# Performance work log

Measured on AMD Instinct MI355X. Metric: run time of the kernel, lower is better.

Reference implementation:

```python
import jax, jax.numpy as jnp
import numpy as np


def rotate_half(x):
    d = x.shape[-1] // 2
    return jnp.concatenate([-x[..., d:], x[..., :d]], axis=-1)


def setup_inputs() -> dict:
    key = jax.random.key(0)
    ks = jax.random.split(key, 8)
    B, T, C, H = 2, 2048, 2048, 16
    hd = C // H
    x = jax.random.normal(ks[0], (B, T, C), dtype=jnp.float32)
    # realistic RoPE tables
    inv_freq = 1.0 / (10000.0 ** (jnp.arange(0, hd, 2, dtype=jnp.float32) / hd))
    t = jnp.arange(T, dtype=jnp.float32)
    freqs = jnp.einsum('t,f->tf', t, inv_freq)
    emb = jnp.concatenate([freqs, freqs], axis=-1)  # [T, hd]
    cos = jnp.cos(emb)
    sin = jnp.sin(emb)
    mask = jnp.tril(jnp.ones((T, T), dtype=bool))[None, None]  # causal [1,1,T,T]
    s = C ** -0.5
    Wq = jax.random.normal(ks[1], (C, C), dtype=jnp.float32) * s
    Wk = jax.random.normal(ks[2], (C, C), dtype=jnp.float32) * s
    Wv = jax.random.normal(ks[3], (C, C), dtype=jnp.float32) * s
    Wo = jax.random.normal(ks[4], (C, C), dtype=jnp.float32) * s
    return {"x": x, "cos": cos, "sin": sin, "mask": mask,
            "Wq": Wq, "Wk": Wk, "Wv": Wv, "Wo": Wo}


def reference(x, cos, sin, mask, Wq, Wk, Wv, Wo):
    B, T, C = x.shape
    H = 16
    hd = C // H
    scale = hd ** -0.5
    # projections: torch Linear stores W as [out,in], y = x @ W^T
    def proj(W):
        return jnp.einsum('btc,dc->btd', x, W).reshape(B, T, H, hd).transpose(0, 2, 1, 3)
    q, k, v = proj(Wq), proj(Wk), proj(Wv)  # [B,H,T,hd]
    c = cos[None, None]  # [1,1,T,hd]
    s = sin[None, None]
    q = q * c + rotate_half(q) * s
    k = k * c + rotate_half(k) * s
    attn = jnp.einsum('bhqd,bhkd->bhqk', q, k) * scale
    attn = jnp.where(mask, attn, -jnp.inf)
    attn = jax.nn.softmax(attn, axis=-1)
    out = jnp.einsum('bhqk,bhkd->bhqd', attn, v)
    out = out.transpose(0, 2, 1, 3).reshape(B, T, C)
    return jnp.einsum('btc,dc->btd', out, Wo)
```

## Files before the change

kernel.cpp:

```cpp
#include <hip/hip_runtime.h>
#include <cstdint>

typedef __bf16 bf16_t;
typedef __bf16 bf16x8 __attribute__((ext_vector_type(8)));
typedef __bf16 bf16x4 __attribute__((ext_vector_type(4)));
typedef float  f32x4  __attribute__((ext_vector_type(4)));

#define BB 2
#define TT 2048
#define CC 2048
#define HH 16
#define HD 128

static __device__ __forceinline__ void async_copy16(const void* gp, void* lp) {
  __builtin_amdgcn_global_load_lds(
      (const __attribute__((address_space(1))) void*)(uintptr_t)gp,
      (__attribute__((address_space(3))) void*)(uint32_t)(uintptr_t)lp,
      16, 0, 0);
}

__global__ __launch_bounds__(256)
void cast_all(const float* __restrict__ x, const float* __restrict__ wq,
              const float* __restrict__ wk, const float* __restrict__ wv,
              const float* __restrict__ wo, bf16_t* __restrict__ xb,
              bf16_t* __restrict__ wq_b) {
  const int NX4 = (BB * TT * CC) / 4;
  const int NW4 = (CC * CC) / 4;
  int i = blockIdx.x * 256 + threadIdx.x;
  const float* s;
  bf16_t* d;
  int off;
  if (i < NX4) {
    s = x; d = xb; off = i;
  } else {
    int j = i - NX4;
    int w = j >> 20;
    off = j & (NW4 - 1);
    s = (w == 0) ? wq : (w == 1) ? wk : (w == 2) ? wv : wo;
    d = wq_b + (size_t)w * (CC * CC);
  }
  float4 v = ((const float4*)s)[off];
  bf16x4 o;
  o[0] = (bf16_t)v.x; o[1] = (bf16_t)v.y; o[2] = (bf16_t)v.z; o[3] = (bf16_t)v.w;
  ((bf16x4*)d)[off] = o;
}

template <int MODE>
__global__ __launch_bounds__(256)
void gemm_bt(const bf16_t* __restrict__ A, const bf16_t* __restrict__ Bw,
             void* __restrict__ C0, void* __restrict__ C1, void* __restrict__ C2,
             int Kdim, int Ndim) {
  __shared__ __align__(16) char smem[128 * 136 * 2];
  bf16_t* As = (bf16_t*)smem;
  bf16_t* Bs = (bf16_t*)(smem + 16384);
  const int tid  = threadIdx.x;
  const int wave = tid >> 6, lane = tid & 63;
  const int quad = lane >> 4, l16 = lane & 15;
  const int m0 = blockIdx.y * 128, n0 = blockIdx.x * 128;
  const int wm = (wave >> 1) * 64, wn = (wave & 1) * 64;

  f32x4 acc[4][4] = {};

  const int srow = lane >> 3;
  const int scol = (((lane & 7) ^ srow) & 7) * 8;
  const int swz  = (l16 & 7) * 8;

  for (int k0 = 0; k0 < Kdim; k0 += 64) {
#pragma unroll
    for (int i = 0; i < 4; ++i) {
      int chunk = wave * 4 + i;
      int row = chunk * 8 + srow;
      async_copy16(A + (size_t)(m0 + row) * Kdim + k0 + scol, As + chunk * 512);
    }
#pragma unroll
    for (int i = 0; i < 4; ++i) {
      int chunk = wave * 4 + i;
      int row = chunk * 8 + srow;
      async_copy16(Bw + (size_t)(n0 + row) * Kdim + k0 + scol, Bs + chunk * 512);
    }
    __syncthreads();
#pragma unroll
    for (int kk = 0; kk < 64; kk += 32) {
      const int koff = (kk + quad * 8) ^ swz;
      bf16x8 af[4], bfr[4];
#pragma unroll
      for (int i = 0; i < 4; ++i)
        af[i] = *(const bf16x8*)&As[(wm + i * 16 + l16) * 64 + koff];
#pragma unroll
      for (int j = 0; j < 4; ++j)
        bfr[j] = *(const bf16x8*)&Bs[(wn + j * 16 + l16) * 64 + koff];
#pragma unroll
      for (int i = 0; i < 4; ++i)
#pragma unroll
        for (int j = 0; j < 4; ++j)
          acc[i][j] = __builtin_amdgcn_mfma_f32_16x16x32_bf16(af[i], bfr[j], acc[i][j], 0, 0, 0);
    }
    __syncthreads();
  }

  if (MODE == 0) {
#pragma unroll
    for (int i = 0; i < 4; ++i)
#pragma unroll
      for (int j = 0; j < 4; ++j) {
        int gcol = n0 + wn + j * 16 + l16;
#pragma unroll
        for (int r = 0; r < 4; ++r) {
          int grow = m0 + wm + i * 16 + quad * 4 + r;
          ((float*)C0)[(size_t)grow * Ndim + gcol] = acc[i][j][r];
        }
      }
  } else {
    const int h = (n0 & (CC - 1)) >> 7;
    bf16_t* Ct = (bf16_t*)smem;
    __syncthreads();
#pragma unroll
    for (int i = 0; i < 4; ++i)
#pragma unroll
      for (int j = 0; j < 4; ++j) {
        int c = wn + j * 16 + l16;
#pragma unroll
        for (int r = 0; r < 4; ++r)
          Ct[(wm + i * 16 + quad * 4 + r) * 136 + c] = (bf16_t)acc[i][j][r];
      }
    __syncthreads();
    const unsigned short* Cu = (const unsigned short*)Ct;
    int col = tid >> 1;
    int rh  = (tid & 1) * 64;
    int grow0 = m0 + rh;
    int b = grow0 >> 11, t0 = grow0 & (TT - 1);
    unsigned int pk[32];
#pragma unroll
    for (int s = 0; s < 32; ++s) {
      unsigned int lo = Cu[(rh + 2 * s) * 136 + col];
      unsigned int hi = Cu[(rh + 2 * s + 1) * 136 + col];
      pk[s] = lo | (hi << 16);
    }
    bf16_t* dstp = (bf16_t*)C2 + ((size_t)(b * HH + h) * HD + col) * TT + t0;
#pragma unroll
    for (int u = 0; u < 8; ++u) {
      uint4 w; w.x = pk[4*u]; w.y = pk[4*u+1]; w.z = pk[4*u+2]; w.w = pk[4*u+3];
      *(uint4*)(dstp + 8 * u) = w;
    }
  }
}

__global__ __launch_bounds__(512, 2)
void gemm_qkv256(const bf16_t* __restrict__ A, const bf16_t* __restrict__ Bw,
                 bf16_t* __restrict__ Qo, bf16_t* __restrict__ Ko,
                 const float* __restrict__ cosT, const float* __restrict__ sinT,
                 int Kdim) {
  extern __shared__ __align__(16) char smem[];
  bf16_t* lds = (bf16_t*)smem;
  const int tid  = threadIdx.x;
  const int wave = tid >> 6, lane = tid & 63;
  const int quad = lane >> 4, l16 = lane & 15;
  const int wm = wave >> 2, wn = wave & 3;
  const int n0 = blockIdx.x * 256, m0 = blockIdx.y * 256;

  const int srow = lane >> 3;
  const int scol = ((lane & 7) ^ srow) * 8;
  const int swz  = (l16 & 7) * 8;
  const int nK = Kdim >> 6;

  const bf16_t* Ag = A  + (size_t)(m0 + wave * 32 + srow) * Kdim + scol;
  const bf16_t* Bg = Bw + (size_t)(n0 + wave * 32 + srow) * Kdim + scol;
  const int ldsChunk = wave * 4 * 512;

#define STAGE_A(kt, buf)                                                      \
  {                                                                           \
    bf16_t* dstA = lds + (buf) * 32768 + ldsChunk;                            \
    const bf16_t* srcA = Ag + (kt) * 64;                                      \
    _Pragma("unroll")                                                         \
    for (int ci = 0; ci < 4; ++ci)                                            \
      async_copy16(srcA + (size_t)(ci * 8) * Kdim, dstA + ci * 512);          \
  }
#define STAGE_B(kt, buf)                                                      \
  {                                                                           \
    bf16_t* dstB = lds + (buf) * 32768 + 16384 + ldsChunk;                    \
    const bf16_t* srcB = Bg + (kt) * 64;                                      \
    _Pragma("unroll")                                                         \
    for (int ci = 0; ci < 4; ++ci)                                            \
      async_copy16(srcB + (size_t)(ci * 8) * Kdim, dstB + ci * 512);          \
  }

  f32x4 acc[8][4] = {};

  STAGE_A(0, 0); STAGE_B(0, 0); STAGE_A(1, 1); STAGE_B(1, 1);

  const int k0off = (quad * 8) ^ swz;
  const int k1off = (32 + quad * 8) ^ swz;

  for (int k = 0; k < nK; ++k) {
    const int cur = k & 1;
    const bf16_t* Asb = lds + cur * 32768;
    const bf16_t* Bsb = Asb + 16384;
    if (k < nK - 1) asm volatile("s_waitcnt vmcnt(8)" ::: "memory");
    else            asm volatile("s_waitcnt vmcnt(0)" ::: "memory");
    __builtin_amdgcn_s_barrier();
    __builtin_amdgcn_sched_barrier(0);

    bf16x8 a0[8], b0[4], a1[8], b1[4];
#pragma unroll
    for (int i = 0; i < 8; ++i)
      a0[i] = *(const bf16x8*)&Asb[(wm * 128 + i * 16 + l16) * 64 + k0off];
#pragma unroll
    for (int j = 0; j < 4; ++j)
      b0[j] = *(const bf16x8*)&Bsb[(wn * 64 + j * 16 + l16) * 64 + k0off];
    asm volatile("s_waitcnt lgkmcnt(0)" ::: "memory");
    __builtin_amdgcn_sched_barrier(0);
    __builtin_amdgcn_s_setprio(1);
#pragma unroll
    for (int i = 0; i < 4; ++i)
#pragma unroll
      for (int j = 0; j < 4; ++j)
        acc[i][j] = __builtin_amdgcn_mfma_f32_16x16x32_bf16(a0[i], b0[j], acc[i][j], 0, 0, 0);
    __builtin_amdgcn_s_setprio(0);

#pragma unroll
    for (int i = 0; i < 8; ++i)
// ... 53 lines not shown
    const int lane16 = tid & 15;
    const int slot0  = tid >> 4;
    const int d0 = lane16 * 8;
    const int dp = d0 ^ 64;
    const float sgn = (d0 < 64) ? -1.f : 1.f;
    const int b = m0 >> 11;
    const int hbase = (n0 & (CC - 1)) >> 7;
#pragma unroll
    for (int p = 0; p < 16; ++p) {
      int gslot = p * 32 + slot0;
      int rowl = gslot >> 1, hh = gslot & 1;
      int t = (m0 + rowl) & (TT - 1);
      const bf16_t* src = Ct + rowl * 268 + hh * 132;
      bf16x8 self = *(const bf16x8*)(src + d0);
      bf16x8 part = *(const bf16x8*)(src + dp);
      const float* ct = cosT + t * HD + d0;
      const float* st = sinT + t * HD + d0;
      float4 c0 = *(const float4*)(ct);
      float4 c1 = *(const float4*)(ct + 4);
      float4 s0 = *(const float4*)(st);
      float4 s1 = *(const float4*)(st + 4);
      float cc[8] = {c0.x, c0.y, c0.z, c0.w, c1.x, c1.y, c1.z, c1.w};
      float ss[8] = {s0.x, s0.y, s0.z, s0.w, s1.x, s1.y, s1.z, s1.w};
      bf16x8 o8;
#pragma unroll
      for (int e = 0; e < 8; ++e)
        o8[e] = (bf16_t)((float)self[e] * cc[e] + sgn * (float)part[e] * ss[e]);
      *(bf16x8*)(dst + (((size_t)(b * HH + hbase + hh) * TT + t) * HD) + d0) = o8;
    }
  }
}

__global__ __launch_bounds__(512, 2)
void attn_kernel(const bf16_t* __restrict__ Q, const bf16_t* __restrict__ K,
                 const bf16_t* __restrict__ Vt, bf16_t* __restrict__ Out) {
  __shared__ __align__(16) bf16_t Ks[2][64 * 128];
  __shared__ __align__(16) bf16_t Vs[2][128 * 64];
  __shared__ __align__(16) bf16_t Pl[8][16 * 76];
  const int lane = threadIdx.x & 63, wave = threadIdx.x >> 6;
  const int quad = lane >> 4, l16 = lane & 15;
  const int linear = blockIdx.x;
  const int hb = linear & 31;
  const int h = hb & (HH - 1), b = hb >> 4;
  const int spair = linear >> 5;
  const size_t qkbase = (size_t)(b * HH + h) * TT * HD;
  const bf16_t* Kh = K + qkbase;
  const bf16_t* Vh = Vt + (size_t)(b * HH + h) * HD * TT;
  const float scale = 0.08838834764831845f;

  const int srK = lane >> 4;
  const int sgK = lane & 15;
  const int scK0 = (sgK ^ srK) * 8;
  const int scK1 = (sgK ^ (4 + srK)) * 8;
  const int srV = lane >> 3;
  const int scV = (((lane & 7) ^ srV) & 7) * 8;
  const int swz = (l16 & 7) * 8;

#pragma unroll
  for (int half = 0; half < 2; ++half) {
    const int qt = half == 0 ? (15 - spair) : spair;
    const int q0 = qt * 128 + wave * 16;
    const int nIter = qt * 2 + 2;

    bf16x8 qf[4];
    {
      const bf16_t* qrow = Q + qkbase + (size_t)(q0 + l16) * HD;
#pragma unroll
      for (int kc = 0; kc < 4; ++kc) qf[kc] = *(const bf16x8*)(qrow + kc * 32 + quad * 8);
    }

    f32x4 o[8] = {};
    float l_i[4] = {};

    {
#pragma unroll
      for (int i = 0; i < 2; ++i) {
        int chunk = wave * 2 + i;
        int sc = (chunk & 1) ? scK1 : scK0;
        async_copy16(Kh + (size_t)(chunk * 4 + srK) * HD + sc, &Ks[0][chunk * 512]);
      }
#pragma unroll
      for (int i = 0; i < 2; ++i) {
        int chunk = wave * 2 + i;
        async_copy16(Vh + (size_t)(chunk * 8 + srV) * TT + scV, &Vs[0][chunk * 512]);
      }
    }

    for (int it = 0; it < nIter; ++it) {
      const int cur = it & 1;
      const int key0 = it * 64;
      __syncthreads();

      if (it + 1 < nIter) {
        const int nxt = cur ^ 1;
        const int knxt = key0 + 64;
#pragma unroll
        for (int i = 0; i < 2; ++i) {
          int chunk = wave * 2 + i;
          int sc = (chunk & 1) ? scK1 : scK0;
          async_copy16(Kh + (size_t)(knxt + chunk * 4 + srK) * HD + sc, &Ks[nxt][chunk * 512]);
        }
#pragma unroll
        for (int i = 0; i < 2; ++i) {
          int chunk = wave * 2 + i;
          async_copy16(Vh + (size_t)(chunk * 8 + srV) * TT + knxt + scV, &Vs[nxt][chunk * 512]);
        }
      }

      f32x4 s[4] = {};
#pragma unroll
      for (int kc = 0; kc < 4; ++kc) {
        const int koff = (kc * 32 + quad * 8) ^ swz;
#pragma unroll
        for (int kt = 0; kt < 4; ++kt) {
          bf16x8 kf = *(const bf16x8*)&Ks[cur][(kt * 16 + l16) * 128 + koff];
          s[kt] = __builtin_amdgcn_mfma_f32_16x16x32_bf16(qf[kc], kf, s[kt], 0, 0, 0);
        }
      }

      {
        bf16_t* pl = &Pl[wave][0];
#pragma unroll
        for (int r = 0; r < 4; ++r) {
          int rel = q0 + quad * 4 + r - key0;
          int prow = (quad * 4 + r) * 76;
          float lr = 0.f;
#pragma unroll
          for (int kt = 0; kt < 4; ++kt) {
            int c16 = kt * 16 + l16;
            float e = (c16 > rel) ? 0.f : __expf(s[kt][r] * scale);
            lr += e;
            pl[prow + c16] = (bf16_t)e;
          }
          l_i[r] += lr;
        }
      }

      bf16x8 pf0 = *(const bf16x8*)&Pl[wave][l16 * 76 + quad * 8];
      bf16x8 pf1 = *(const bf16x8*)&Pl[wave][l16 * 76 + 32 + quad * 8];
      const int voff0 = (quad * 8) ^ swz;
      const int voff1 = (32 + quad * 8) ^ swz;
#pragma unroll
      for (int n = 0; n < 8; ++n) {
        bf16x8 vf0 = *(const bf16x8*)&Vs[cur][(n * 16 + l16) * 64 + voff0];
        bf16x8 vf1 = *(const bf16x8*)&Vs[cur][(n * 16 + l16) * 64 + voff1];
        o[n] = __builtin_amdgcn_mfma_f32_16x16x32_bf16(pf0, vf0, o[n], 0, 0, 0);
        o[n] = __builtin_amdgcn_mfma_f32_16x16x32_bf16(pf1, vf1, o[n], 0, 0, 0);
      }
    }

#pragma unroll
    for (int r = 0; r < 4; ++r) {
      float l = l_i[r];
#pragma unroll
      for (int off = 1; off < 16; off <<= 1) l += __shfl_xor(l, off);
      l_i[r] = 1.f / l;
    }

#pragma unroll
    for (int n = 0; n < 8; ++n)
#pragma unroll
      for (int r = 0; r < 4; ++r) {
        int qg = q0 + quad * 4 + r;
        size_t off = ((size_t)(b * TT + qg) * CC) + h * HD + n * 16 + l16;
        Out[off] = (bf16_t)(o[n][r] * l_i[r]);
      }
  }
}

extern "C" void kernel_launch(void* const* d_in, const int* in_sizes, int n_in,
                              void* d_out, int out_size, void* d_ws, size_t ws_size,
                              hipStream_t stream) {
  const float* x    = (const float*)d_in[0];
  const float* cosT = (const float*)d_in[1];
  const float* sinT = (const float*)d_in[2];
  const float* Wq = (const float*)d_in[4];
  const float* Wk = (const float*)d_in[5];
  const float* Wv = (const float*)d_in[6];
  const float* Wo = (const float*)d_in[7];
  float* out = (float*)d_out;

  char* ws = (char*)d_ws;
  const size_t XSZ = (size_t)BB * TT * CC * 2;
  const size_t WSZ = (size_t)CC * CC * 2;
  bf16_t* x_bf  = (bf16_t*)(ws);
  bf16_t* wq_bf = (bf16_t*)(ws + XSZ);
  bf16_t* wv_bf = (bf16_t*)(ws + XSZ + 2 * WSZ);
  bf16_t* wo_bf = (bf16_t*)(ws + XSZ + 3 * WSZ);
  bf16_t* Qb    = (bf16_t*)(ws + XSZ + 4 * WSZ);
  bf16_t* Kb    = (bf16_t*)(ws + 2 * XSZ + 4 * WSZ);
  bf16_t* Vt    = (bf16_t*)(ws + 3 * XSZ + 4 * WSZ);
  bf16_t* attn_bf = x_bf;

  const int NX = BB * TT * CC;
  const int NW = CC * CC;
  cast_all<<<(NX / 4 + 4 * (NW / 4)) / 256, 256, 0, stream>>>(
      x, Wq, Wk, Wv, Wo, x_bf, wq_bf);

  (void)hipFuncSetAttribute(reinterpret_cast<const void*>(gemm_qkv256),
                            hipFuncAttributeMaxDynamicSharedMemorySize, 137216);
  gemm_qkv256<<<dim3(2 * CC / 256, BB * TT / 256), 512, 137216, stream>>>(
      x_bf, wq_bf, Qb, Kb, cosT, sinT, CC);

  gemm_bt<1><<<dim3(CC / 128, BB * TT / 128), 256, 0, stream>>>(
      x_bf, wv_bf, nullptr, nullptr, Vt, CC, CC);

  attn_kernel<<<dim3(BB * HH * 8), 512, 0, stream>>>(Qb, Kb, Vt, attn_bf);

  gemm_bt<0><<<dim3(CC / 128, BB * TT / 128), 256, 0, stream>>>(
      attn_bf, wo_bf, out, nullptr, nullptr, CC, CC);
}
```

Measured before the change: 369.2 us.

## Fuse all stages into one cooperative persistent kernel with grid syncs

Replaces the five separate launches (cast, QK projection with RoPE, V projection, attention, output projection) with a single cooperative kernel of 256 blocks that runs each stage in turn, separated by grid-wide syncs. The goal is to remove per-launch overhead and inter-kernel gaps. In exchange, every stage is pinned to a fixed 256-block, 512-thread grid that may fit some stages poorly, grid syncs add their own cost, and the V and Wo GEMMs use a simpler single-barrier pipeline. If the cooperative launch fails, the original multi-kernel path runs instead.

```diff
diff --git a/kernel.cpp b/kernel.cpp
--- a/kernel.cpp
+++ b/kernel.cpp
@@ -1,5 +1,8 @@
 #include <hip/hip_runtime.h>
+#include <hip/hip_cooperative_groups.h>
 #include <cstdint>
+
+namespace cg = cooperative_groups;
 
 typedef __bf16 bf16_t;
 typedef __bf16 bf16x8 __attribute__((ext_vector_type(8)));
@@ -18,6 +21,7 @@
       (__attribute__((address_space(3))) void*)(uint32_t)(uintptr_t)lp,
       16, 0, 0);
 }
+
 
 __global__ __launch_bounds__(256)
 void cast_all(const float* __restrict__ x, const float* __restrict__ wq,
@@ -185,7 +189,6 @@
   }
 
   f32x4 acc[8][4] = {};
-
   STAGE_A(0, 0); STAGE_B(0, 0); STAGE_A(1, 1); STAGE_B(1, 1);
 
   const int k0off = (quad * 8) ^ swz;
@@ -441,6 +444,467 @@
   }
 }
 
+__global__ __launch_bounds__(512, 2)
+void mega_kernel(const float* __restrict__ x, const float* __restrict__ cosT,
+                 const float* __restrict__ sinT, const float* __restrict__ Wqf,
+                 const float* __restrict__ Wkf, const float* __restrict__ Wvf,
+                 const float* __restrict__ Wof, bf16_t* __restrict__ xb,
+                 bf16_t* __restrict__ wq_b, bf16_t* __restrict__ Qb,
+                 bf16_t* __restrict__ Kb, bf16_t* __restrict__ Vt,
+                 float* __restrict__ out) {
+  extern __shared__ __align__(16) char smem[];
+  bf16_t* lds = (bf16_t*)smem;
+  const int bid = blockIdx.x;
+  const int tid = threadIdx.x;
+  const int wave = tid >> 6, lane = tid & 63;
+  const int quad = lane >> 4, l16 = lane & 15;
+  const int srow = lane >> 3;
+  const int scol = ((lane & 7) ^ srow) * 8;
+  const int swz  = (l16 & 7) * 8;
+
+  {
+    const int NX4 = (BB * TT * CC) / 4;
+    const int NW4 = (CC * CC) / 4;
+    const int total = NX4 + 4 * NW4;
+    for (int i = bid * 512 + tid; i < total; i += 256 * 512) {
+      const float* s; bf16_t* d; int off;
+      if (i < NX4) { s = x; d = xb; off = i; }
+      else {
+        int j = i - NX4; int w = j >> 20; off = j & (NW4 - 1);
+        s = (w == 0) ? Wqf : (w == 1) ? Wkf : (w == 2) ? Wvf : Wof;
+        d = wq_b + (size_t)w * (CC * CC);
+      }
+      float4 v = ((const float4*)s)[off];
+      bf16x4 o;
+      o[0] = (bf16_t)v.x; o[1] = (bf16_t)v.y; o[2] = (bf16_t)v.z; o[3] = (bf16_t)v.w;
+      ((bf16x4*)d)[off] = o;
+    }
+  }
+  __threadfence();
+  cg::this_grid().sync();
+
+  {
+    const int n0 = (bid & 15) * 256, m0 = (bid >> 4) * 256;
+    const int wm = wave >> 2, wn = wave & 3;
+    const int nK = CC >> 6;
+    const bf16_t* Ag = xb   + (size_t)(m0 + wave * 32 + srow) * CC + scol;
+    const bf16_t* Bg = wq_b + (size_t)(n0 + wave * 32 + srow) * CC + scol;
+    const int ldsChunk = wave * 2048;
+
+#define QSTAGE_A(kt, buf)                                                     \
+  {                                                                           \
+    bf16_t* dstA = lds + (buf) * 32768 + ldsChunk;                            \
+    const bf16_t* srcA = Ag + (kt) * 64;                                      \
+    _Pragma("unroll")                                                         \
+    for (int ci = 0; ci < 4; ++ci)                                            \
+      async_copy16(srcA + (size_t)(ci * 8) * CC, dstA + ci * 512);            \
+  }
+#define QSTAGE_B(kt, buf)                                                     \
+  {                                                                           \
+    bf16_t* dstB = lds + (buf) * 32768 + 16384 + ldsChunk;                    \
+    const bf16_t* srcB = Bg + (kt) * 64;                                      \
+    _Pragma("unroll")                                                         \
+    for (int ci = 0; ci < 4; ++ci)                                            \
+      async_copy16(srcB + (size_t)(ci * 8) * CC, dstB + ci * 512);            \
+  }
+
+    f32x4 acc[8][4] = {};
+    QSTAGE_A(0, 0); QSTAGE_B(0, 0); QSTAGE_A(1, 1); QSTAGE_B(1, 1);
+
+    const int k0off = (quad * 8) ^ swz;
+    const int k1off = (32 + quad * 8) ^ swz;
+
+    for (int k = 0; k < nK; ++k) {
+      const int cur = k & 1;
+      const bf16_t* Asb = lds + cur * 32768;
+      const bf16_t* Bsb = Asb + 16384;
+      if (k < nK - 1) asm volatile("s_waitcnt vmcnt(8)" ::: "memory");
+      else            asm volatile("s_waitcnt vmcnt(0)" ::: "memory");
+      __builtin_amdgcn_s_barrier();
+      __builtin_amdgcn_sched_barrier(0);
+
+      bf16x8 a0[8], b0[4], a1[8], b1[4];
+#pragma unroll
+      for (int i = 0; i < 8; ++i)
+        a0[i] = *(const bf16x8*)&Asb[(wm * 128 + i * 16 + l16) * 64 + k0off];
+#pragma unroll
+      for (int j = 0; j < 4; ++j)
+        b0[j] = *(const bf16x8*)&Bsb[(wn * 64 + j * 16 + l16) * 64 + k0off];
+      asm volatile("s_waitcnt lgkmcnt(0)" ::: "memory");
+      __builtin_amdgcn_sched_barrier(0);
+      __builtin_amdgcn_s_setprio(1);
+#pragma unroll
+      for (int i = 0; i < 4; ++i)
+#pragma unroll
+        for (int j = 0; j < 4; ++j)
+          acc[i][j] = __builtin_amdgcn_mfma_f32_16x16x32_bf16(a0[i], b0[j], acc[i][j], 0, 0, 0);
+      __builtin_amdgcn_s_setprio(0);
+
+#pragma unroll
+      for (int i = 0; i < 8; ++i)
+        a1[i] = *(const bf16x8*)&Asb[(wm * 128 + i * 16 + l16) * 64 + k1off];
+#pragma unroll
+      for (int j = 0; j < 4; ++j)
+        b1[j] = *(const bf16x8*)&Bsb[(wn * 64 + j * 16 + l16) * 64 + k1off];
+      __builtin_amdgcn_s_setprio(1);
+#pragma unroll
+      for (int i = 4; i < 8; ++i)
+#pragma unroll
+        for (int j = 0; j < 4; ++j)
+          acc[i][j] = __builtin_amdgcn_mfma_f32_16x16x32_bf16(a0[i], b0[j], acc[i][j], 0, 0, 0);
+      __builtin_amdgcn_s_setprio(0);
+      asm volatile("s_waitcnt lgkmcnt(0)" ::: "memory");
+      __builtin_amdgcn_s_barrier();
+      __builtin_amdgcn_sched_barrier(0);
+
+      if (k + 2 < nK) QSTAGE_A(k + 2, cur);
+      __builtin_amdgcn_s_setprio(1);
+#pragma unroll
+      for (int i = 0; i < 4; ++i)
+#pragma unroll
+        for (int j = 0; j < 4; ++j)
+          acc[i][j] = __builtin_amdgcn_mfma_f32_16x16x32_bf16(a1[i], b1[j], acc[i][j], 0, 0, 0);
+      __builtin_amdgcn_s_setprio(0);
+
+      if (k + 2 < nK) QSTAGE_B(k + 2, cur);
+      __builtin_amdgcn_s_setprio(1);
+#pragma unroll
+      for (int i = 4; i < 8; ++i)
+#pragma unroll
+        for (int j = 0; j < 4; ++j)
+          acc[i][j] = __builtin_amdgcn_mfma_f32_16x16x32_bf16(a1[i], b1[j], acc[i][j], 0, 0, 0);
+      __builtin_amdgcn_s_setprio(0);
+    }
+#undef QSTAGE_A
+#undef QSTAGE_B
+
+    {
+      const int proj = n0 >> 11;
+      bf16_t* dst = proj == 0 ? Qb : Kb;
+      bf16_t* Ct = lds;
+#pragma unroll
+      for (int i = 0; i < 8; ++i)
+#pragma unroll
+        for (int j = 0; j < 4; ++j) {
+          int coll = wn * 64 + j * 16 + l16;
+          int pcol = coll + ((coll >> 7) << 2);
+#pragma unroll
+          for (int r = 0; r < 4; ++r) {
+            int rowl = wm * 128 + i * 16 + quad * 4 + r;
+            Ct[rowl * 268 + pcol] = (bf16_t)acc[i][j][r];
+          }
+        }
+      __syncthreads();
+      const int lane16 = tid & 15;
+      const int slot0  = tid >> 4;
+      const int d0 = lane16 * 8;
+      const int dp = d0 ^ 64;
+      const float sgn = (d0 < 64) ? -1.f : 1.f;
+      const int b = m0 >> 11;
+      const int hbase = (n0 & (CC - 1)) >> 7;
+#pragma unroll
+      for (int p = 0; p < 16; ++p) {
+        int gslot = p * 32 + slot0;
+        int rowl = gslot >> 1, hh = gslot & 1;
+        int t = (m0 + rowl) & (TT - 1);
+        const bf16_t* src = Ct + rowl * 268 + hh * 132;
+        bf16x8 self = *(const bf16x8*)(src + d0);
+        bf16x8 part = *(const bf16x8*)(src + dp);
+        const float* ct = cosT + t * HD + d0;
+        const float* st = sinT + t * HD + d0;
+        float4 c0 = *(const float4*)(ct);
+        float4 c1 = *(const float4*)(ct + 4);
+        float4 s0 = *(const float4*)(st);
+        float4 s1 = *(const float4*)(st + 4);
+        float cc[8] = {c0.x, c0.y, c0.z, c0.w, c1.x, c1.y, c1.z, c1.w};
+        float ss[8] = {s0.x, s0.y, s0.z, s0.w, s1.x, s1.y, s1.z, s1.w};
+        bf16x8 o8;
+#pragma unroll
+        for (int e = 0; e < 8; ++e)
+          o8[e] = (bf16_t)((float)self[e] * cc[e] + sgn * (float)part[e] * ss[e]);
+        *(bf16x8*)(dst + (((size_t)(b * HH + hbase + hh) * TT + t) * HD) + d0) = o8;
+      }
+    }
+  }
+  __syncthreads();
+
+  {
+    const int m0 = (bid & 31) * 128;
+    const int n0v = (bid >> 5) * 256;
+    const bf16_t* Bv = wq_b + 2 * (size_t)CC * CC;
+    const int wmv = (wave >> 2) * 64, wnv = (wave & 3) * 64;
+    const int nK = CC >> 6;
+    f32x4 acc[4][4] = {};
+
+#define VSTG(kt, buf) do {                                                    \
+    bf16_t* base_ = lds + (buf) * 24576;                                      \
+    _Pragma("unroll")                                                         \
+    for (int c_ = 0; c_ < 2; ++c_) {                                          \
+      int ch_ = wave * 2 + c_;                                                \
+      async_copy16(xb + (size_t)(m0 + ch_ * 8 + srow) * CC + (kt) * 64 + scol,\
+                   base_ + ch_ * 512);                                        \
+    }                                                                         \
+    _Pragma("unroll")                                                         \
+    for (int c_ = 0; c_ < 4; ++c_) {                                          \
+      int ch_ = wave * 4 + c_;                                                \
+      async_copy16(Bv + (size_t)(n0v + ch_ * 8 + srow) * CC + (kt) * 64 + scol,\
+                   base_ + 8192 + ch_ * 512);                                 \
+    }                                                                         \
+  } while (0)
+
+    VSTG(0, 0);
+    for (int k = 0; k < nK; ++k) {
+      __syncthreads();
+      if (k + 1 < nK) VSTG(k + 1, (k + 1) & 1);
+      const bf16_t* As = lds + (k & 1) * 24576;
+      const bf16_t* Bs = As + 8192;
+#pragma unroll
+      for (int kk = 0; kk < 64; kk += 32) {
+        const int koff = (kk + quad * 8) ^ swz;
+        bf16x8 af[4], bfr[4];
+#pragma unroll
+        for (int i = 0; i < 4; ++i)
+          af[i] = *(const bf16x8*)&As[(wmv + i * 16 + l16) * 64 + koff];
+#pragma unroll
+        for (int j = 0; j < 4; ++j)
+          bfr[j] = *(const bf16x8*)&Bs[(wnv + j * 16 + l16) * 64 + koff];
+#pragma unroll
+        for (int i = 0; i < 4; ++i)
+#pragma unroll
+          for (int j = 0; j < 4; ++j)
+            acc[i][j] = __builtin_amdgcn_mfma_f32_16x16x32_bf16(af[i], bfr[j], acc[i][j], 0, 0, 0);
+      }
+    }
+#undef VSTG
+    __syncthreads();
+    {
+      bf16_t* Ct = lds;
+#pragma unroll
+      for (int i = 0; i < 4; ++i)
+#pragma unroll
+        for (int j = 0; j < 4; ++j) {
+          int c = wnv + j * 16 + l16;
+#pragma unroll
+          for (int r = 0; r < 4; ++r)
+            Ct[(wmv + i * 16 + quad * 4 + r) * 264 + c] = (bf16_t)acc[i][j][r];
+        }
+      __syncthreads();
+      const unsigned short* Cu = (const unsigned short*)Ct;
+      int col = tid >> 1;
+      int rh  = (tid & 1) * 64;
+      int dv = n0v + col;
+      int h = dv >> 7, d = dv & (HD - 1);
+      int b = m0 >> 11;
+      int t0 = (m0 & (TT - 1)) + rh;
+      unsigned int pk[32];
+#pragma unroll
+      for (int s = 0; s < 32; ++s) {
+        unsigned int lo = Cu[(rh + 2 * s) * 264 + col];
+        unsigned int hi = Cu[(rh + 2 * s + 1) * 264 + col];
+        pk[s] = lo | (hi << 16);
+      }
+      bf16_t* dstp = Vt + ((size_t)(b * HH + h) * HD + d) * TT + t0;
+#pragma unroll
+      for (int u = 0; u < 8; ++u) {
+        uint4 w; w.x = pk[4*u]; w.y = pk[4*u+1]; w.z = pk[4*u+2]; w.w = pk[4*u+3];
+        *(uint4*)(dstp + 8 * u) = w;
+      }
+    }
+  }
+  __threadfence();
+  cg::this_grid().sync();
+
+  {
+    bf16_t* KsL = lds;
+    bf16_t* VsL = lds + 16384;
+    bf16_t* PlW = lds + 32768 + wave * 1216;
+    const int hb = bid & 31;
+    const int h = hb & (HH - 1), b = hb >> 4;
+    const int spair = bid >> 5;
+    const size_t qkbase = (size_t)(b * HH + h) * TT * HD;
+    const bf16_t* Kh = Kb + qkbase;
+    const bf16_t* Vh = Vt + (size_t)(b * HH + h) * HD * TT;
+    const float scale = 0.08838834764831845f;
+    const int srK = lane >> 4;
+    const int sgK = lane & 15;
+    const int scK0 = (sgK ^ srK) * 8;
+    const int scK1 = (sgK ^ (4 + srK)) * 8;
+    const int srV = lane >> 3;
+    const int scV = (((lane & 7) ^ srV) & 7) * 8;
+
+#pragma unroll
+    for (int half = 0; half < 2; ++half) {
+      const int qt = half == 0 ? (15 - spair) : spair;
+      const int q0 = qt * 128 + wave * 16;
+      const int nIter = qt * 2 + 2;
+
+      bf16x8 qf[4];
+      {
+        const bf16_t* qrow = Qb + qkbase + (size_t)(q0 + l16) * HD;
+#pragma unroll
+        for (int kc = 0; kc < 4; ++kc) qf[kc] = *(const bf16x8*)(qrow + kc * 32 + quad * 8);
+      }
+
+      f32x4 o[8] = {};
+      float l_i[4] = {};
+
+#pragma unroll
+      for (int i2 = 0; i2 < 2; ++i2) {
+        int chunk = wave * 2 + i2;
+        int sc = (chunk & 1) ? scK1 : scK0;
+        async_copy16(Kh + (size_t)(chunk * 4 + srK) * HD + sc, KsL + chunk * 512);
+      }
+#pragma unroll
+      for (int i2 = 0; i2 < 2; ++i2) {
+        int chunk = wave * 2 + i2;
+        async_copy16(Vh + (size_t)(chunk * 8 + srV) * TT + scV, VsL + chunk * 512);
+      }
+
+      for (int it = 0; it < nIter; ++it) {
+        const int cur = it & 1;
+        const int key0 = it * 64;
+        __syncthreads();
+
+        if (it + 1 < nIter) {
+          const int nxt = cur ^ 1;
+          const int knxt = key0 + 64;
+#pragma unroll
+          for (int i2 = 0; i2 < 2; ++i2) {
+            int chunk = wave * 2 + i2;
+            int sc = (chunk & 1) ? scK1 : scK0;
+            async_copy16(Kh + (size_t)(knxt + chunk * 4 + srK) * HD + sc,
+                         KsL + nxt * 8192 + chunk * 512);
+          }
+#pragma unroll
+          for (int i2 = 0; i2 < 2; ++i2) {
+            int chunk = wave * 2 + i2;
+            async_copy16(Vh + (size_t)(chunk * 8 + srV) * TT + knxt + scV,
+                         VsL + nxt * 8192 + chunk * 512);
+          }
+        }
+
+        f32x4 s4[4] = {};
+#pragma unroll
+        for (int kc = 0; kc < 4; ++kc) {
+          const int koff = (kc * 32 + quad * 8) ^ swz;
+#pragma unroll
+          for (int kt = 0; kt < 4; ++kt) {
+            bf16x8 kf = *(const bf16x8*)&KsL[cur * 8192 + (kt * 16 + l16) * 128 + koff];
+            s4[kt] = __builtin_amdgcn_mfma_f32_16x16x32_bf16(qf[kc], kf, s4[kt], 0, 0, 0);
+          }
+        }
+
+#pragma unroll
+        for (int r = 0; r < 4; ++r) {
+          int rel = q0 + quad * 4 + r - key0;
+          int prow = (quad * 4 + r) * 76;
+          float lr = 0.f;
+#pragma unroll
+          for (int kt = 0; kt < 4; ++kt) {
+            int c16 = kt * 16 + l16;
+            float e = (c16 > rel) ? 0.f : __expf(s4[kt][r] * scale);
+            lr += e;
+            PlW[prow + c16] = (bf16_t)e;
+          }
+          l_i[r] += lr;
+        }
+
+        bf16x8 pf0 = *(const bf16x8*)(PlW + l16 * 76 + quad * 8);
+        bf16x8 pf1 = *(const bf16x8*)(PlW + l16 * 76 + 32 + quad * 8);
+        const int voff0 = (quad * 8) ^ swz;
+        const int voff1 = (32 + quad * 8) ^ swz;
+#pragma unroll
+        for (int n = 0; n < 8; ++n) {
+          bf16x8 vf0 = *(const bf16x8*)&VsL[cur * 8192 + (n * 16 + l16) * 64 + voff0];
+          bf16x8 vf1 = *(const bf16x8*)&VsL[cur * 8192 + (n * 16 + l16) * 64 + voff1];
+          o[n] = __builtin_amdgcn_mfma_f32_16x16x32_bf16(pf0, vf0, o[n], 0, 0, 0);
+          o[n] = __builtin_amdgcn_mfma_f32_16x16x32_bf16(pf1, vf1, o[n], 0, 0, 0);
+        }
+      }
+
+#pragma unroll
+      for (int r = 0; r < 4; ++r) {
+        float l = l_i[r];
+#pragma unroll
+        for (int off = 1; off < 16; off <<= 1) l += __shfl_xor(l, off);
+        l_i[r] = 1.f / l;
+      }
+
+#pragma unroll
+      for (int n = 0; n < 8; ++n)
+#pragma unroll
+        for (int r = 0; r < 4; ++r) {
+          int qg = q0 + quad * 4 + r;
+          size_t off = ((size_t)(b * TT + qg) * CC) + h * HD + n * 16 + l16;
+          xb[off] = (bf16_t)(o[n][r] * l_i[r]);
+        }
+    }
+  }
+  __threadfence();
+  cg::this_grid().sync();
+
+  {
+    const int m0 = (bid & 31) * 128;
+    const int n0w = (bid >> 5) * 256;
+    const bf16_t* Bw2 = wq_b + 3 * (size_t)CC * CC;
+    const int wmv = (wave >> 2) * 64, wnv = (wave & 3) * 64;
+    const int nK = CC >> 6;
+    f32x4 acc[4][4] = {};
+
+#define WSTG(kt, buf) do {                                                    \
+    bf16_t* base_ = lds + (buf) * 24576;                                      \
+    _Pragma("unroll")                                                         \
+    for (int c_ = 0; c_ < 2; ++c_) {                                          \
+      int ch_ = wave * 2 + c_;                                                \
+      async_copy16(xb + (size_t)(m0 + ch_ * 8 + srow) * CC + (kt) * 64 + scol,\
+                   base_ + ch_ * 512);                                        \
+    }                                                                         \
+    _Pragma("unroll")                                                         \
+    for (int c_ = 0; c_ < 4; ++c_) {                                          \
+      int ch_ = wave * 4 + c_;                                                \
+      async_copy16(Bw2 + (size_t)(n0w + ch_ * 8 + srow) * CC + (kt) * 64 + scol,\
+                   base_ + 8192 + ch_ * 512);                                 \
+    }                                                                         \
+  } while (0)
+
+    WSTG(0, 0);
+    for (int k = 0; k < nK; ++k) {
+      __syncthreads();
+      if (k + 1 < nK) WSTG(k + 1, (k + 1) & 1);
+      const bf16_t* As = lds + (k & 1) * 24576;
+      const bf16_t* Bs = As + 8192;
+#pragma unroll
+      for (int kk = 0; kk < 64; kk += 32) {
+        const int koff = (kk + quad * 8) ^ swz;
+        bf16x8 af[4], bfr[4];
+#pragma unroll
+        for (int i = 0; i < 4; ++i)
+          af[i] = *(const bf16x8*)&As[(wmv + i * 16 + l16) * 64 + koff];
+#pragma unroll
+        for (int j = 0; j < 4; ++j)
+          bfr[j] = *(const bf16x8*)&Bs[(wnv + j * 16 + l16) * 64 + koff];
+#pragma unroll
+        for (int i = 0; i < 4; ++i)
+#pragma unroll
+          for (int j = 0; j < 4; ++j)
+            acc[i][j] = __builtin_amdgcn_mfma_f32_16x16x32_bf16(af[i], bfr[j], acc[i][j], 0, 0, 0);
+      }
+    }
+#undef WSTG
+#pragma unroll
+    for (int i = 0; i < 4; ++i)
+#pragma unroll
+      for (int j = 0; j < 4; ++j) {
+        int gcol = n0w + wnv + j * 16 + l16;
+#pragma unroll
+        for (int r = 0; r < 4; ++r) {
+          int grow = m0 + wmv + i * 16 + quad * 4 + r;
+          out[(size_t)grow * CC + gcol] = acc[i][j][r];
+        }
+      }
+  }
+}
+
 extern "C" void kernel_launch(void* const* d_in, const int* in_sizes, int n_in,
                               void* d_out, int out_size, void* d_ws, size_t ws_size,
                               hipStream_t stream) {
@@ -465,21 +929,29 @@
   bf16_t* Vt    = (bf16_t*)(ws + 3 * XSZ + 4 * WSZ);
   bf16_t* attn_bf = x_bf;
 
-  const int NX = BB * TT * CC;
-  const int NW = CC * CC;
-  cast_all<<<(NX / 4 + 4 * (NW / 4)) / 256, 256, 0, stream>>>(
-      x, Wq, Wk, Wv, Wo, x_bf, wq_bf);
-
+  (void)hipFuncSetAttribute(reinterpret_cast<const void*>(mega_kernel),
+                            hipFuncAttributeMaxDynamicSharedMemorySize, 137216);
   (void)hipFuncSetAttribute(reinterpret_cast<const void*>(gemm_qkv256),
                             hipFuncAttributeMaxDynamicSharedMemorySize, 137216);
-  gemm_qkv256<<<dim3(2 * CC / 256, BB * TT / 256), 512, 137216, stream>>>(
-      x_bf, wq_bf, Qb, Kb, cosT, sinT, CC);
-
-  gemm_bt<1><<<dim3(CC / 128, BB * TT / 128), 256, 0, stream>>>(
-      x_bf, wv_bf, nullptr, nullptr, Vt, CC, CC);
-
-  attn_kernel<<<dim3(BB * HH * 8), 512, 0, stream>>>(Qb, Kb, Vt, attn_bf);
-
-  gemm_bt<0><<<dim3(CC / 128, BB * TT / 128), 256, 0, stream>>>(
-      attn_bf, wo_bf, out, nullptr, nullptr, CC, CC);
+
+  void* args[] = {(void*)&x,  (void*)&cosT, (void*)&sinT, (void*)&Wq,
+                  (void*)&Wk, (void*)&Wv,   (void*)&Wo,   (void*)&x_bf,
+                  (void*)&wq_bf, (void*)&Qb, (void*)&Kb,  (void*)&Vt,
+                  (void*)&out};
+  hipError_t err = hipLaunchCooperativeKernel(
+      mega_kernel, dim3(256), dim3(512), args, 137216, stream);
+
+  if (err != hipSuccess) {
+    const int NX = BB * TT * CC;
+    const int NW = CC * CC;
+    cast_all<<<(NX / 4 + 4 * (NW / 4)) / 256, 256, 0, stream>>>(
+        x, Wq, Wk, Wv, Wo, x_bf, wq_bf);
+    gemm_qkv256<<<dim3(2 * CC / 256, BB * TT / 256), 512, 137216, stream>>>(
+        x_bf, wq_bf, Qb, Kb, cosT, sinT, CC);
+    gemm_bt<1><<<dim3(CC / 128, BB * TT / 128), 256, 0, stream>>>(
+        x_bf, wv_bf, nullptr, nullptr, Vt, CC, CC);
+    attn_kernel<<<dim3(BB * HH * 8), 512, 0, stream>>>(Qb, Kb, Vt, attn_bf);
+    gemm_bt<0><<<dim3(CC / 128, BB * TT / 128), 256, 0, stream>>>(
+        attn_bf, wo_bf, out, nullptr, nullptr, CC, CC);
+  }
 }
```

New measurement: 700.3 us. 1.9x slower.

## Restructure attention to 32-row waves and add pipelined Wo GEMM kernel

Applied to the files above, without the earlier changes.

Two changes. First, the attention kernel moves from 8 waves each handling 16 query rows over two paired query tiles to 4 waves each handling 32 rows (two 16-row M-tiles) of one tile per block. This reuses every K/V fragment loaded from LDS for two MFMAs, and the P buffer gets an XOR swizzle instead of padding. Second, the output projection drops the simple 128x128 GEMM for a 128x256, 512-thread, double-buffered async-copy kernel with interleaved MFMA/load scheduling and setprio hints. The cost is more registers per wave, a grid of 512 blocks of varying causal length that may be less balanced than the old paired scheme, and a larger LDS footprint for the Wo GEMM.

```diff
diff --git a/kernel.cpp b/kernel.cpp
--- a/kernel.cpp
+++ b/kernel.cpp
@@ -45,11 +45,9 @@
   ((bf16x4*)d)[off] = o;
 }
 
-template <int MODE>
 __global__ __launch_bounds__(256)
-void gemm_bt(const bf16_t* __restrict__ A, const bf16_t* __restrict__ Bw,
-             void* __restrict__ C0, void* __restrict__ C1, void* __restrict__ C2,
-             int Kdim, int Ndim) {
+void gemm_v(const bf16_t* __restrict__ A, const bf16_t* __restrict__ Bw,
+            bf16_t* __restrict__ C2, int Kdim) {
   __shared__ __align__(16) char smem[128 * 136 * 2];
   bf16_t* As = (bf16_t*)smem;
   bf16_t* Bs = (bf16_t*)(smem + 16384);
@@ -98,50 +96,36 @@
     __syncthreads();
   }
 
-  if (MODE == 0) {
-#pragma unroll
-    for (int i = 0; i < 4; ++i)
-#pragma unroll
-      for (int j = 0; j < 4; ++j) {
-        int gcol = n0 + wn + j * 16 + l16;
-#pragma unroll
-        for (int r = 0; r < 4; ++r) {
-          int grow = m0 + wm + i * 16 + quad * 4 + r;
-          ((float*)C0)[(size_t)grow * Ndim + gcol] = acc[i][j][r];
-        }
-      }
-  } else {
-    const int h = (n0 & (CC - 1)) >> 7;
-    bf16_t* Ct = (bf16_t*)smem;
-    __syncthreads();
-#pragma unroll
-    for (int i = 0; i < 4; ++i)
-#pragma unroll
-      for (int j = 0; j < 4; ++j) {
-        int c = wn + j * 16 + l16;
-#pragma unroll
-        for (int r = 0; r < 4; ++r)
-          Ct[(wm + i * 16 + quad * 4 + r) * 136 + c] = (bf16_t)acc[i][j][r];
-      }
-    __syncthreads();
-    const unsigned short* Cu = (const unsigned short*)Ct;
-    int col = tid >> 1;
-    int rh  = (tid & 1) * 64;
-    int grow0 = m0 + rh;
-    int b = grow0 >> 11, t0 = grow0 & (TT - 1);
-    unsigned int pk[32];
-#pragma unroll
-    for (int s = 0; s < 32; ++s) {
-      unsigned int lo = Cu[(rh + 2 * s) * 136 + col];
-      unsigned int hi = Cu[(rh + 2 * s + 1) * 136 + col];
-      pk[s] = lo | (hi << 16);
-    }
-    bf16_t* dstp = (bf16_t*)C2 + ((size_t)(b * HH + h) * HD + col) * TT + t0;
-#pragma unroll
-    for (int u = 0; u < 8; ++u) {
-      uint4 w; w.x = pk[4*u]; w.y = pk[4*u+1]; w.z = pk[4*u+2]; w.w = pk[4*u+3];
-      *(uint4*)(dstp + 8 * u) = w;
-    }
+  const int h = (n0 & (CC - 1)) >> 7;
+  bf16_t* Ct = (bf16_t*)smem;
+  __syncthreads();
+#pragma unroll
+  for (int i = 0; i < 4; ++i)
+#pragma unroll
+    for (int j = 0; j < 4; ++j) {
+      int c = wn + j * 16 + l16;
+#pragma unroll
+      for (int r = 0; r < 4; ++r)
+        Ct[(wm + i * 16 + quad * 4 + r) * 136 + c] = (bf16_t)acc[i][j][r];
+    }
+  __syncthreads();
+  const unsigned short* Cu = (const unsigned short*)Ct;
+  int col = tid >> 1;
+  int rh  = (tid & 1) * 64;
+  int grow0 = m0 + rh;
+  int b = grow0 >> 11, t0 = grow0 & (TT - 1);
+  unsigned int pk[32];
+#pragma unroll
+  for (int s = 0; s < 32; ++s) {
+    unsigned int lo = Cu[(rh + 2 * s) * 136 + col];
+    unsigned int hi = Cu[(rh + 2 * s + 1) * 136 + col];
+    pk[s] = lo | (hi << 16);
+  }
+  bf16_t* dstp = C2 + ((size_t)(b * HH + h) * HD + col) * TT + t0;
+#pragma unroll
+  for (int u = 0; u < 8; ++u) {
+    uint4 w; w.x = pk[4*u]; w.y = pk[4*u+1]; w.z = pk[4*u+2]; w.w = pk[4*u+3];
+    *(uint4*)(dstp + 8 * u) = w;
   }
 }
 
@@ -185,7 +169,6 @@
   }
 
   f32x4 acc[8][4] = {};
-
   STAGE_A(0, 0); STAGE_B(0, 0); STAGE_A(1, 1); STAGE_B(1, 1);
 
   const int k0off = (quad * 8) ^ swz;
@@ -305,17 +288,138 @@
 }
 
 __global__ __launch_bounds__(512, 2)
+void gemm_wo(const bf16_t* __restrict__ A, const bf16_t* __restrict__ Bw,
+             float* __restrict__ C, int Kdim) {
+  extern __shared__ __align__(16) char smem[];
+  bf16_t* lds = (bf16_t*)smem;
+  const int tid  = threadIdx.x;
+  const int wave = tid >> 6, lane = tid & 63;
+  const int quad = lane >> 4, l16 = lane & 15;
+  const int wm = wave >> 2, wn = wave & 3;
+  const int n0 = blockIdx.x * 256, m0 = blockIdx.y * 128;
+
+  const int srow = lane >> 3;
+  const int scol = ((lane & 7) ^ srow) * 8;
+  const int swz  = (l16 & 7) * 8;
+  const int nK = Kdim >> 6;
+
+#define WSTAGE_A(kt, buf)                                                     \
+  {                                                                           \
+    bf16_t* d_ = lds + (buf) * 24576;                                         \
+    _Pragma("unroll")                                                         \
+    for (int c_ = 0; c_ < 2; ++c_) {                                          \
+      int ch_ = wave * 2 + c_;                                                \
+      async_copy16(A + (size_t)(m0 + ch_ * 8 + srow) * Kdim + (kt) * 64 + scol,\
+                   d_ + ch_ * 512);                                           \
+    }                                                                         \
+  }
+#define WSTAGE_B(kt, buf)                                                     \
+  {                                                                           \
+    bf16_t* d_ = lds + (buf) * 24576 + 8192;                                  \
+    _Pragma("unroll")                                                         \
+    for (int c_ = 0; c_ < 4; ++c_) {                                          \
+      int ch_ = wave * 4 + c_;                                                \
+      async_copy16(Bw + (size_t)(n0 + ch_ * 8 + srow) * Kdim + (kt) * 64 + scol,\
+                   d_ + ch_ * 512);                                           \
+    }                                                                         \
+  }
+
+  f32x4 acc[4][4] = {};
+  WSTAGE_A(0, 0); WSTAGE_B(0, 0); WSTAGE_A(1, 1); WSTAGE_B(1, 1);
+
+  const int k0off = (quad * 8) ^ swz;
+  const int k1off = (32 + quad * 8) ^ swz;
+
+  for (int k = 0; k < nK; ++k) {
+    const int cur = k & 1;
+    const bf16_t* As = lds + cur * 24576;
+    const bf16_t* Bs = As + 8192;
+    if (k < nK - 1) asm volatile("s_waitcnt vmcnt(6)" ::: "memory");
+    else            asm volatile("s_waitcnt vmcnt(0)" ::: "memory");
+    __builtin_amdgcn_s_barrier();
+    __builtin_amdgcn_sched_barrier(0);
+
+    bf16x8 a0[4], b0[4], a1[4], b1[4];
+#pragma unroll
+    for (int i = 0; i < 4; ++i)
+      a0[i] = *(const bf16x8*)&As[(wm * 64 + i * 16 + l16) * 64 + k0off];
+#pragma unroll
+    for (int j = 0; j < 4; ++j)
+      b0[j] = *(const bf16x8*)&Bs[(wn * 64 + j * 16 + l16) * 64 + k0off];
+    asm volatile("s_waitcnt lgkmcnt(0)" ::: "memory");
+    __builtin_amdgcn_sched_barrier(0);
+    __builtin_amdgcn_s_setprio(1);
+#pragma unroll
+    for (int i = 0; i < 4; ++i)
+#pragma unroll
+      for (int j = 0; j < 2; ++j)
+        acc[i][j] = __builtin_amdgcn_mfma_f32_16x16x32_bf16(a0[i], b0[j], acc[i][j], 0, 0, 0);
+    __builtin_amdgcn_s_setprio(0);
+
+#pragma unroll
+    for (int i = 0; i < 4; ++i)
+      a1[i] = *(const bf16x8*)&As[(wm * 64 + i * 16 + l16) * 64 + k1off];
+#pragma unroll
+    for (int j = 0; j < 4; ++j)
+      b1[j] = *(const bf16x8*)&Bs[(wn * 64 + j * 16 + l16) * 64 + k1off];
+    __builtin_amdgcn_s_setprio(1);
+#pragma unroll
+    for (int i = 0; i < 4; ++i)
+#pragma unroll
+      for (int j = 2; j < 4; ++j)
+        acc[i][j] = __builtin_amdgcn_mfma_f32_16x16x32_bf16(a0[i], b0[j], acc[i][j], 0, 0, 0);
+    __builtin_amdgcn_s_setprio(0);
+    asm volatile("s_waitcnt lgkmcnt(0)" ::: "memory");
+    __builtin_amdgcn_s_barrier();
+    __builtin_amdgcn_sched_barrier(0);
+
+    if (k + 2 < nK) WSTAGE_A(k + 2, cur);
+    __builtin_amdgcn_s_setprio(1);
+#pragma unroll
+    for (int i = 0; i < 4; ++i)
+#pragma unroll
+      for (int j = 0; j < 2; ++j)
+        acc[i][j] = __builtin_amdgcn_mfma_f32_16x16x32_bf16(a1[i], b1[j], acc[i][j], 0, 0, 0);
+    __builtin_amdgcn_s_setprio(0);
+
+    if (k + 2 < nK) WSTAGE_B(k + 2, cur);
+    __builtin_amdgcn_s_setprio(1);
+#pragma unroll
+    for (int i = 0; i < 4; ++i)
+#pragma unroll
+      for (int j = 2; j < 4; ++j)
+        acc[i][j] = __builtin_amdgcn_mfma_f32_16x16x32_bf16(a1[i], b1[j], acc[i][j], 0, 0, 0);
+    __builtin_amdgcn_s_setprio(0);
+  }
+#undef WSTAGE_A
+#undef WSTAGE_B
+
+#pragma unroll
+  for (int i = 0; i < 4; ++i)
+#pragma unroll
+    for (int j = 0; j < 4; ++j) {
+      int gcol = n0 + wn * 64 + j * 16 + l16;
+#pragma unroll
+      for (int r = 0; r < 4; ++r) {
+        int grow = m0 + wm * 64 + i * 16 + quad * 4 + r;
+        C[(size_t)grow * CC + gcol] = acc[i][j][r];
+      }
+    }
+}
+
+__global__ __launch_bounds__(256, 2)
 void attn_kernel(const bf16_t* __restrict__ Q, const bf16_t* __restrict__ K,
                  const bf16_t* __restrict__ Vt, bf16_t* __restrict__ Out) {
   __shared__ __align__(16) bf16_t Ks[2][64 * 128];
   __shared__ __align__(16) bf16_t Vs[2][128 * 64];
-  __shared__ __align__(16) bf16_t Pl[8][16 * 76];
+  __shared__ __align__(16) bf16_t Pl[4][2][16 * 64];
   const int lane = threadIdx.x & 63, wave = threadIdx.x >> 6;
   const int quad = lane >> 4, l16 = lane & 15;
   const int linear = blockIdx.x;
   const int hb = linear & 31;
   const int h = hb & (HH - 1), b = hb >> 4;
-  const int spair = linear >> 5;
+  const int qt = (TT / 128 - 1) - (linear >> 5);
+  const int q0 = qt * 128 + wave * 32;
   const size_t qkbase = (size_t)(b * HH + h) * TT * HD;
   const bf16_t* Kh = K + qkbase;
   const bf16_t* Vh = Vt + (size_t)(b * HH + h) * HD * TT;
@@ -328,117 +432,128 @@
   const int srV = lane >> 3;
   const int scV = (((lane & 7) ^ srV) & 7) * 8;
   const int swz = (l16 & 7) * 8;
-
-#pragma unroll
-  for (int half = 0; half < 2; ++half) {
-    const int qt = half == 0 ? (15 - spair) : spair;
-    const int q0 = qt * 128 + wave * 16;
-    const int nIter = qt * 2 + 2;
-
-    bf16x8 qf[4];
-    {
-      const bf16_t* qrow = Q + qkbase + (size_t)(q0 + l16) * HD;
-#pragma unroll
-      for (int kc = 0; kc < 4; ++kc) qf[kc] = *(const bf16x8*)(qrow + kc * 32 + quad * 8);
-    }
-
-    f32x4 o[8] = {};
-    float l_i[4] = {};
-
-    {
-#pragma unroll
-      for (int i = 0; i < 2; ++i) {
-        int chunk = wave * 2 + i;
+  const int psw = (l16 & 7) << 3;
+
+  bf16x8 qf[2][4];
+#pragma unroll
+  for (int mt = 0; mt < 2; ++mt) {
+    const bf16_t* qrow = Q + qkbase + (size_t)(q0 + mt * 16 + l16) * HD;
+#pragma unroll
+    for (int kc = 0; kc < 4; ++kc) qf[mt][kc] = *(const bf16x8*)(qrow + kc * 32 + quad * 8);
+  }
+
+  f32x4 o[2][8] = {};
+  float l_i[2][4] = {};
+
+  const int nIter = qt * 2 + 2;
+
+  {
+#pragma unroll
+    for (int i = 0; i < 4; ++i) {
+      int chunk = wave * 4 + i;
+      int sc = (chunk & 1) ? scK1 : scK0;
+      async_copy16(Kh + (size_t)(chunk * 4 + srK) * HD + sc, &Ks[0][chunk * 512]);
+    }
+#pragma unroll
+    for (int i = 0; i < 4; ++i) {
+      int chunk = wave * 4 + i;
+      async_copy16(Vh + (size_t)(chunk * 8 + srV) * TT + scV, &Vs[0][chunk * 512]);
+    }
+  }
+
+  for (int it = 0; it < nIter; ++it) {
+    const int cur = it & 1;
+    const int key0 = it * 64;
+    __syncthreads();
+
+    if (it + 1 < nIter) {
+      const int nxt = cur ^ 1;
+      const int knxt = key0 + 64;
+#pragma unroll
+      for (int i = 0; i < 4; ++i) {
+        int chunk = wave * 4 + i;
         int sc = (chunk & 1) ? scK1 : scK0;
-        async_copy16(Kh + (size_t)(chunk * 4 + srK) * HD + sc, &Ks[0][chunk * 512]);
+        async_copy16(Kh + (size_t)(knxt + chunk * 4 + srK) * HD + sc, &Ks[nxt][chunk * 512]);
       }
 #pragma unroll
-      for (int i = 0; i < 2; ++i) {
-        int chunk = wave * 2 + i;
-        async_copy16(Vh + (size_t)(chunk * 8 + srV) * TT + scV, &Vs[0][chunk * 512]);
+      for (int i = 0; i < 4; ++i) {
+        int chunk = wave * 4 + i;
+        async_copy16(Vh + (size_t)(chunk * 8 + srV) * TT + knxt + scV, &Vs[nxt][chunk * 512]);
       }
     }
 
-    for (int it = 0; it < nIter; ++it) {
-      const int cur = it & 1;
-      const int key0 = it * 64;
-      __syncthreads();
-
-      if (it + 1 < nIter) {
-        const int nxt = cur ^ 1;
-        const int knxt = key0 + 64;
-#pragma unroll
-        for (int i = 0; i < 2; ++i) {
-          int chunk = wave * 2 + i;
-          int sc = (chunk & 1) ? scK1 : scK0;
-          async_copy16(Kh + (size_t)(knxt + chunk * 4 + srK) * HD + sc, &Ks[nxt][chunk * 512]);
+    f32x4 s[2][4] = {};
+#pragma unroll
+    for (int kc = 0; kc < 4; ++kc) {
+      const int koff = (kc * 32 + quad * 8) ^ swz;
+#pragma unroll
+      for (int kt = 0; kt < 4; ++kt) {
+        bf16x8 kf = *(const bf16x8*)&Ks[cur][(kt * 16 + l16) * 128 + koff];
+        s[0][kt] = __builtin_amdgcn_mfma_f32_16x16x32_bf16(qf[0][kc], kf, s[0][kt], 0, 0, 0);
+        s[1][kt] = __builtin_amdgcn_mfma_f32_16x16x32_bf16(qf[1][kc], kf, s[1][kt], 0, 0, 0);
+      }
+    }
+
+#pragma unroll
+    for (int mt = 0; mt < 2; ++mt) {
+      bf16_t* pl = &Pl[wave][mt][0];
+#pragma unroll
+      for (int r = 0; r < 4; ++r) {
+        int prow = quad * 4 + r;
+        int rel = q0 + mt * 16 + prow - key0;
+        int rbase = prow * 64;
+        int sw = (prow & 7) << 3;
+        float lr = 0.f;
+#pragma unroll
+        for (int kt = 0; kt < 4; ++kt) {
+          int c16 = kt * 16 + l16;
+          float e = (c16 > rel) ? 0.f : __expf(s[mt][kt][r] * scale);
+          lr += e;
+          pl[rbase + (c16 ^ sw)] = (bf16_t)e;
         }
-#pragma unroll
-        for (int i = 0; i < 2; ++i) {
-          int chunk = wave * 2 + i;
-          async_copy16(Vh + (size_t)(chunk * 8 + srV) * TT + knxt + scV, &Vs[nxt][chunk * 512]);
-        }
+        l_i[mt][r] += lr;
       }
-
-      f32x4 s[4] = {};
-#pragma unroll
-      for (int kc = 0; kc < 4; ++kc) {
-        const int koff = (kc * 32 + quad * 8) ^ swz;
-#pragma unroll
-        for (int kt = 0; kt < 4; ++kt) {
-          bf16x8 kf = *(const bf16x8*)&Ks[cur][(kt * 16 + l16) * 128 + koff];
-          s[kt] = __builtin_amdgcn_mfma_f32_16x16x32_bf16(qf[kc], kf, s[kt], 0, 0, 0);
-        }
+    }
+
+    bf16x8 pf[2][2];
+#pragma unroll
+    for (int mt = 0; mt < 2; ++mt) {
+      pf[mt][0] = *(const bf16x8*)&Pl[wave][mt][l16 * 64 + ((quad * 8) ^ psw)];
+      pf[mt][1] = *(const bf16x8*)&Pl[wave][mt][l16 * 64 + ((32 + quad * 8) ^ psw)];
+    }
+    const int voff0 = (quad * 8) ^ swz;
+    const int voff1 = (32 + quad * 8) ^ swz;
+#pragma unroll
+    for (int n = 0; n < 8; ++n) {
+      bf16x8 vf0 = *(const bf16x8*)&Vs[cur][(n * 16 + l16) * 64 + voff0];
+      bf16x8 vf1 = *(const bf16x8*)&Vs[cur][(n * 16 + l16) * 64 + voff1];
+      o[0][n] = __builtin_amdgcn_mfma_f32_16x16x32_bf16(pf[0][0], vf0, o[0][n], 0, 0, 0);
+      o[0][n] = __builtin_amdgcn_mfma_f32_16x16x32_bf16(pf[0][1], vf1, o[0][n], 0, 0, 0);
+      o[1][n] = __builtin_amdgcn_mfma_f32_16x16x32_bf16(pf[1][0], vf0, o[1][n], 0, 0, 0);
+      o[1][n] = __builtin_amdgcn_mfma_f32_16x16x32_bf16(pf[1][1], vf1, o[1][n], 0, 0, 0);
+    }
+  }
+
+#pragma unroll
+  for (int mt = 0; mt < 2; ++mt)
+#pragma unroll
+    for (int r = 0; r < 4; ++r) {
+      float l = l_i[mt][r];
+#pragma unroll
+      for (int off = 1; off < 16; off <<= 1) l += __shfl_xor(l, off);
+      l_i[mt][r] = 1.f / l;
+    }
+
+#pragma unroll
+  for (int mt = 0; mt < 2; ++mt)
+#pragma unroll
+    for (int n = 0; n < 8; ++n)
+#pragma unroll
+      for (int r = 0; r < 4; ++r) {
+        int qg = q0 + mt * 16 + quad * 4 + r;
+        size_t off = ((size_t)(b * TT + qg) * CC) + h * HD + n * 16 + l16;
+        Out[off] = (bf16_t)(o[mt][n][r] * l_i[mt][r]);
       }
-
-      {
-        bf16_t* pl = &Pl[wave][0];
-#pragma unroll
-        for (int r = 0; r < 4; ++r) {
-          int rel = q0 + quad * 4 + r - key0;
-          int prow = (quad * 4 + r) * 76;
-          float lr = 0.f;
-#pragma unroll
-          for (int kt = 0; kt < 4; ++kt) {
-            int c16 = kt * 16 + l16;
-            float e = (c16 > rel) ? 0.f : __expf(s[kt][r] * scale);
-            lr += e;
-            pl[prow + c16] = (bf16_t)e;
-          }
-          l_i[r] += lr;
-        }
-      }
-
-      bf16x8 pf0 = *(const bf16x8*)&Pl[wave][l16 * 76 + quad * 8];
-      bf16x8 pf1 = *(const bf16x8*)&Pl[wave][l16 * 76 + 32 + quad * 8];
-      const int voff0 = (quad * 8) ^ swz;
-      const int voff1 = (32 + quad * 8) ^ swz;
-#pragma unroll
-      for (int n = 0; n < 8; ++n) {
-        bf16x8 vf0 = *(const bf16x8*)&Vs[cur][(n * 16 + l16) * 64 + voff0];
-        bf16x8 vf1 = *(const bf16x8*)&Vs[cur][(n * 16 + l16) * 64 + voff1];
-        o[n] = __builtin_amdgcn_mfma_f32_16x16x32_bf16(pf0, vf0, o[n], 0, 0, 0);
-        o[n] = __builtin_amdgcn_mfma_f32_16x16x32_bf16(pf1, vf1, o[n], 0, 0, 0);
-      }
-    }
-
-#pragma unroll
-    for (int r = 0; r < 4; ++r) {
-      float l = l_i[r];
-#pragma unroll
-      for (int off = 1; off < 16; off <<= 1) l += __shfl_xor(l, off);
-      l_i[r] = 1.f / l;
-    }
-
-#pragma unroll
-    for (int n = 0; n < 8; ++n)
-#pragma unroll
-      for (int r = 0; r < 4; ++r) {
-        int qg = q0 + quad * 4 + r;
-        size_t off = ((size_t)(b * TT + qg) * CC) + h * HD + n * 16 + l16;
-        Out[off] = (bf16_t)(o[n][r] * l_i[r]);
-      }
-  }
 }
 
 extern "C" void kernel_launch(void* const* d_in, const int* in_sizes, int n_in,
@@ -475,11 +590,13 @@
   gemm_qkv256<<<dim3(2 * CC / 256, BB * TT / 256), 512, 137216, stream>>>(
       x_bf, wq_bf, Qb, Kb, cosT, sinT, CC);
 
-  gemm_bt<1><<<dim3(CC / 128, BB * TT / 128), 256, 0, stream>>>(
-      x_bf, wv_bf, nullptr, nullptr, Vt, CC, CC);
-
-  attn_kernel<<<dim3(BB * HH * 8), 512, 0, stream>>>(Qb, Kb, Vt, attn_bf);
-
-  gemm_bt<0><<<dim3(CC / 128, BB * TT / 128), 256, 0, stream>>>(
-      attn_bf, wo_bf, out, nullptr, nullptr, CC, CC);
+  gemm_v<<<dim3(CC / 128, BB * TT / 128), 256, 0, stream>>>(
+      x_bf, wv_bf, Vt, CC);
+
+  attn_kernel<<<dim3(BB * HH * (TT / 128)), 256, 0, stream>>>(Qb, Kb, Vt, attn_bf);
+
+  (void)hipFuncSetAttribute(reinterpret_cast<const void*>(gemm_wo),
+                            hipFuncAttributeMaxDynamicSharedMemorySize, 98304);
+  gemm_wo<<<dim3(CC / 256, BB * TT / 128), 512, 98304, stream>>>(
+      attn_bf, wo_bf, out, CC);
 }
```

Result: faster. 359.2 us (-2.7%).
